# Optimization experiments

Hardware: AMD Instinct MI355X
Metric: run time of the kernel (lower is better)

The kernel has to match this reference:

```python
import jax, jax.numpy as jnp
import numpy as np

B, S, D, H = 2, 2048, 1024, 16
DH = D // H


def setup_inputs() -> dict:
    key = jax.random.key(0)
    ks = jax.random.split(key, 12)
    sc = 1.0 / np.sqrt(D)
    return {
        "query": jax.random.normal(ks[0], (B, S, D), jnp.float32),
        "key": jax.random.normal(ks[1], (B, S, D), jnp.float32),
        "value": jax.random.normal(ks[2], (B, S, D), jnp.float32),
        "key_mask": jax.random.randint(ks[3], (B, S), 0, 2, jnp.int32),
        "Wq": jax.random.normal(ks[4], (D, D), jnp.float32) * sc,
        "bq": jnp.zeros((D,), jnp.float32),
        "Wk": jax.random.normal(ks[5], (D, D), jnp.float32) * sc,
        "bk": jnp.zeros((D,), jnp.float32),
        "Wv": jax.random.normal(ks[6], (D, D), jnp.float32) * sc,
        "bv": jnp.zeros((D,), jnp.float32),
        "Wo": jax.random.normal(ks[7], (D, D), jnp.float32) * sc,
        "bo": jnp.zeros((D,), jnp.float32),
    }


def _shape(x):
    # (B, L, D) -> (B, H, L, DH)
    return x.reshape(B, -1, H, DH).transpose(0, 2, 1, 3)


def reference(query, key, value, key_mask, Wq, bq, Wk, bk, Wv, bv, Wo, bo):
    # linear projections (torch Linear: x @ W.T + b)
    q = _shape(query @ Wq.T + bq)  # (B,H,S,DH)
    k = _shape(key @ Wk.T + bk)
    v = _shape(value @ Wv.T + bv)

    q = q / jnp.sqrt(jnp.asarray(DH, q.dtype))
    scores = jnp.einsum("bhqd,bhkd->bhqk", q, k)  # (B,H,S,S)

    pad = (key_mask == 0)[:, None, None, :]  # (B,1,1,K)
    scores = jnp.where(pad, jnp.asarray(-1e18, scores.dtype), scores)
    attn = jax.nn.softmax(scores, axis=-1)
    attn = jnp.where(pad, jnp.asarray(0.0, attn.dtype), attn)
    # dropout p=0.0 (eval) -> identity

    ctx = jnp.einsum("bhqk,bhkd->bhqd", attn, v)
    ctx = ctx.transpose(0, 2, 1, 3).reshape(B, -1, D)  # unshape
    output = ctx @ Wo.T + bo
    return (output, attn)
```

## Files before the change

kernel.cpp:

```cpp
#include <hip/hip_runtime.h>

#define B_  2
#define S_  2048
#define D_  1024
#define H_  16
#define DH_ 64

typedef _Float16 f16;
typedef f16   f16x2 __attribute__((ext_vector_type(2)));
typedef f16   f16x4 __attribute__((ext_vector_type(4)));
typedef f16   f16x8 __attribute__((ext_vector_type(8)));
typedef float f32x4 __attribute__((ext_vector_type(4)));
typedef float f32x16 __attribute__((ext_vector_type(16)));

static __device__ __forceinline__ f16x8 ldsm8(const f16* p) {
    return *reinterpret_cast<const f16x8*>(p);
}

static __device__ __forceinline__ int swz(int row, int byteInRow) {
    return row * 128 + (byteInRow ^ ((row & 7) << 4));
}

static __device__ __forceinline__ void gll16(const void* g, void* l) {
    __builtin_amdgcn_global_load_lds(
        (const __attribute__((address_space(1))) void*)g,
        (__attribute__((address_space(3))) void*)l, 16, 0, 0);
}

static __device__ __forceinline__ unsigned pk16(float a, float b) {
    return __builtin_bit_cast(unsigned, __builtin_amdgcn_cvt_pkrtz(a, b));
}

__global__ __launch_bounds__(256)
void qkv_gemm(const float* __restrict__ Aq, const float* __restrict__ Ak,
              const float* __restrict__ Av,
              const float* __restrict__ Wq, const float* __restrict__ Wk,
              const float* __restrict__ Wv,
              const float* __restrict__ bq, const float* __restrict__ bk,
              const float* __restrict__ bv,
              f16* __restrict__ qo, f16* __restrict__ ko, f16* __restrict__ vo,
              float qscale)
{
    constexpr int K = 1024, N = 1024;
    __shared__ __align__(16) f16 As[128][40];
    __shared__ __align__(16) f16 Bs[128][40];
    const int z = blockIdx.z;
    const float* A    = z == 0 ? Aq : z == 1 ? Ak : Av;
    const float* W    = z == 0 ? Wq : z == 1 ? Wk : Wv;
    const float* bias = z == 0 ? bq : z == 1 ? bk : bv;
    const float scale = z == 0 ? qscale : 1.0f;

    const int t  = threadIdx.x;
    const int bm = blockIdx.y * 128;
    const int bn = blockIdx.x * 128;
    const int w  = t >> 6, l = t & 63;
    const int wr = w >> 1, wc = w & 1;
    const int lr = l & 15, lg = l >> 4;

    f32x4 acc[4][4];
    #pragma unroll
    for (int m = 0; m < 4; ++m)
        #pragma unroll
        for (int n = 0; n < 4; ++n)
            acc[m][n] = (f32x4){0.f, 0.f, 0.f, 0.f};

    for (int kt = 0; kt < K / 32; ++kt) {
        #pragma unroll
        for (int i = 0; i < 4; ++i) {
            int idx = t + i * 256;
            int row = idx >> 3, g = idx & 7;
            float4 v = *reinterpret_cast<const float4*>(A + (size_t)(bm + row) * K + kt * 32 + g * 4);
            alignas(8) f16 hh[4] = {(f16)v.x, (f16)v.y, (f16)v.z, (f16)v.w};
            *reinterpret_cast<uint2*>(&As[row][g * 4]) = *reinterpret_cast<uint2*>(hh);
        }
        #pragma unroll
        for (int i = 0; i < 4; ++i) {
            int idx = t + i * 256;
            int row = idx >> 3, g = idx & 7;
            float4 v = *reinterpret_cast<const float4*>(W + (size_t)(bn + row) * K + kt * 32 + g * 4);
            alignas(8) f16 hh[4] = {(f16)v.x, (f16)v.y, (f16)v.z, (f16)v.w};
            *reinterpret_cast<uint2*>(&Bs[row][g * 4]) = *reinterpret_cast<uint2*>(hh);
        }
        __syncthreads();

        f16x8 af[4], bfv[4];
        #pragma unroll
        for (int m = 0; m < 4; ++m) af[m]  = ldsm8(&As[wr * 64 + m * 16 + lr][lg * 8]);
        #pragma unroll
        for (int n = 0; n < 4; ++n) bfv[n] = ldsm8(&Bs[wc * 64 + n * 16 + lr][lg * 8]);
        #pragma unroll
        for (int m = 0; m < 4; ++m)
            #pragma unroll
            for (int n = 0; n < 4; ++n)
                acc[m][n] = __builtin_amdgcn_mfma_f32_16x16x32_f16(af[m], bfv[n], acc[m][n], 0, 0, 0);
        __syncthreads();
    }

    #pragma unroll
    for (int m = 0; m < 4; ++m) {
        #pragma unroll
        for (int n = 0; n < 4; ++n) {
            int col = bn + wc * 64 + n * 16 + lr;
            float bb = bias[col];
            if (z == 2) {
                int row0 = bm + wr * 64 + m * 16 + lg * 4;
                int b = row0 >> 11, s = row0 & 2047;
                int hh_ = col >> 6, d = col & 63;
                alignas(8) f16 hv[4];
                #pragma unroll
                for (int j = 0; j < 4; ++j)
                    hv[j] = (f16)(acc[m][n][j] + bb);
                *reinterpret_cast<uint2*>(vo +
                    (((size_t)(b * 16 + hh_) * 64 + d) * 2048 + s)) =
                    *reinterpret_cast<uint2*>(hv);
            } else {
                f16* Cp = z == 0 ? qo : ko;
                #pragma unroll
                for (int j = 0; j < 4; ++j) {
                    int row = bm + wr * 64 + m * 16 + lg * 4 + j;
                    Cp[(size_t)row * N + col] = (f16)((acc[m][n][j] + bb) * scale);
                }
            }
        }
    }
}

__global__ __launch_bounds__(256)
void gemm_out(const f16* __restrict__ A, const float* __restrict__ W,
              const float* __restrict__ bias, float* __restrict__ Cp)
{
    constexpr int K = 1024, N = 1024;
    __shared__ __align__(16) f16 As[128][40];
    __shared__ __align__(16) f16 Bs[128][40];
    const int t  = threadIdx.x;
    const int bm = blockIdx.y * 128;
    const int bn = blockIdx.x * 128;
    const int w  = t >> 6, l = t & 63;
    const int wr = w >> 1, wc = w & 1;
    const int lr = l & 15, lg = l >> 4;

    f32x4 acc[4][4];
    #pragma unroll
    for (int m = 0; m < 4; ++m)
        #pragma unroll
        for (int n = 0; n < 4; ++n)
            acc[m][n] = (f32x4){0.f, 0.f, 0.f, 0.f};

    for (int kt = 0; kt < K / 32; ++kt) {
        #pragma unroll
        for (int i = 0; i < 2; ++i) {
            int idx = t + i * 256;
            int row = idx >> 2, g = idx & 3;
            *reinterpret_cast<uint4*>(&As[row][g * 8]) =
                *reinterpret_cast<const uint4*>(A + (size_t)(bm + row) * K + kt * 32 + g * 8);
        }
        #pragma unroll
        for (int i = 0; i < 4; ++i) {
            int idx = t + i * 256;
            int row = idx >> 3, g = idx & 7;
            float4 v = *reinterpret_cast<const float4*>(W + (size_t)(bn + row) * K + kt * 32 + g * 4);
            alignas(8) f16 hh[4] = {(f16)v.x, (f16)v.y, (f16)v.z, (f16)v.w};
            *reinterpret_cast<uint2*>(&Bs[row][g * 4]) = *reinterpret_cast<uint2*>(hh);
        }
        __syncthreads();

        f16x8 af[4], bfv[4];
        #pragma unroll
        for (int m = 0; m < 4; ++m) af[m]  = ldsm8(&As[wr * 64 + m * 16 + lr][lg * 8]);
        #pragma unroll
        for (int n = 0; n < 4; ++n) bfv[n] = ldsm8(&Bs[wc * 64 + n * 16 + lr][lg * 8]);
        #pragma unroll
        for (int m = 0; m < 4; ++m)
            #pragma unroll
            for (int n = 0; n < 4; ++n)
                acc[m][n] = __builtin_amdgcn_mfma_f32_16x16x32_f16(af[m], bfv[n], acc[m][n], 0, 0, 0);
        __syncthreads();
    }

    #pragma unroll
    for (int m = 0; m < 4; ++m) {
        #pragma unroll
        for (int n = 0; n < 4; ++n) {
            int col = bn + wc * 64 + n * 16 + lr;
            float bb = bias[col];
            #pragma unroll
            for (int j = 0; j < 4; ++j) {
                int row = bm + wr * 64 + m * 16 + lg * 4 + j;
                Cp[(size_t)row * N + col] = acc[m][n][j] + bb;
            }
        }
    }
}

__global__ __launch_bounds__(256, 3)
void attn_fused(const f16* __restrict__ qh, const f16* __restrict__ khp,
                const f16* __restrict__ vtg, const int* __restrict__ kmask,
                float* __restrict__ attn_out, f16* __restrict__ ch)
{
    __shared__ __align__(16) f16 ksd[2][64 * 64];
    __shared__ __align__(16) f16 vsd[2][64 * 64];
    __shared__ __align__(16) f16 ps[128][76];
    __shared__ float linv_s[128];
    __shared__ unsigned mbits[64];

    const int t  = threadIdx.x;
    const int w  = t >> 6, l = t & 63, lo = l & 31, hi = l >> 5;
    const bool H1 = (hi == 1);

    const int bid  = blockIdx.x;
    const int xcd  = bid & 7;
    const int slot = bid >> 3;
    const int bh   = (xcd << 2) | (slot >> 4);
    const int qt   = slot & 15;
    const int b    = bh >> 4;
    const int h    = bh & 15;
    const int q0   = qt * 128;
    const int row  = q0 + w * 32 + lo;
    const int lrow = w * 32 + lo;

    f16x8 qf[4];
    {
        const f16* qb = qh + (size_t)(b * S_ + row) * D_ + h * DH_ + hi * 8;
        #pragma unroll
        for (int c = 0; c < 4; ++c) qf[c] = *reinterpret_cast<const f16x8*>(qb + c * 16);
    }

    #pragma unroll
    for (int r = 0; r < 8; ++r) {
        int ktm = w * 8 + r;
        int mkv = kmask[b * S_ + ktm * 64 + l];
        unsigned long long bl = __ballot(mkv != 0);
        if (l == 0) {
            mbits[ktm * 2]     = (unsigned)bl;
            mbits[ktm * 2 + 1] = (unsigned)(bl >> 32);
        }
    }
    asm volatile("s_waitcnt vmcnt(0)" ::: "memory");

    const int r8 = l >> 3, l8 = l & 7;
    const int xorc8 = (l8 ^ r8) * 8;
    const f16* kgb = khp + (size_t)b * S_ * D_ + h * DH_;
    const f16* vgb = vtg + (size_t)(bh * 64) * S_;

    auto stageK128 = [&](int slot2, int jt) {
        char* tb = slot2 ? (char*)&vsd[0][0] : (char*)&ksd[0][0];
        #pragma unroll
        for (int i = 0; i < 4; ++i) {
            int rr = w * 32 + i * 8 + r8;
            gll16(kgb + (size_t)(jt * 128 + rr) * D_ + xorc8,
                  tb + w * 4096 + i * 1024);
        }
    };
    auto stageK = [&](int buf, int kt) {
        #pragma unroll
        for (int i = 0; i < 2; ++i) {
            int rr = i * 32 + w * 8 + r8;
            gll16(kgb + (size_t)(kt * 64 + rr) * D_ + xorc8,
                  (char*)ksd + buf * 8192 + i * 4096 + w * 1024);
        }
    };
    auto stageV = [&](int buf, int kt) {
        #pragma unroll
        for (int i = 0; i < 2; ++i) {
            int rr = i * 32 + w * 8 + r8;
            gll16(vgb + (size_t)rr * S_ + kt * 64 + xorc8,
                  (char*)vsd + buf * 8192 + i * 4096 + w * 1024);
        }
    };

    stageK128(0, 0);
    asm volatile("s_waitcnt vmcnt(0) lgkmcnt(0)" ::: "memory");
    __builtin_amdgcn_s_barrier();

    float ls0 = 0.f, ls1 = 0.f;
    for (int jt = 0; jt < 16; ++jt) {
        if (jt + 1 < 16) stageK128((jt + 1) & 1, jt + 1);
        const char* tb = (jt & 1) ? (const char*)&vsd[0][0] : (const char*)&ksd[0][0];

        #pragma unroll
        for (int h4 = 0; h4 < 4; ++h4) {
            f32x16 s;
            #pragma unroll
            for (int i = 0; i < 16; ++i) s[i] = 0.f;
            #pragma unroll
            for (int c = 0; c < 4; ++c) {
                f16x8 kf = *reinterpret_cast<const f16x8*>(
                    tb + swz(h4 * 32 + lo, c * 32 + hi * 16));
                s = __builtin_amdgcn_mfma_f32_32x32x16_f16(kf, qf[c], s, 0, 0, 0);
            }
            const unsigned m = mbits[jt * 4 + h4] >> (hi * 4);
            #pragma unroll
            for (int q4 = 0; q4 < 4; ++q4)
                #pragma unroll
                for (int j = 0; j < 4; ++j) {
                    float e = __builtin_amdgcn_exp2f(s[q4 * 4 + j]);
                    float z = ((m >> (q4 * 8 + j)) & 1) ? e : 0.0f;
                    if (q4 & 1) ls1 += z; else ls0 += z;
                }
        }
        asm volatile("s_waitcnt vmcnt(0)" ::: "memory");
        __builtin_amdgcn_s_barrier();
    }

    float ls = ls0 + ls1;
    ls += __shfl_xor(ls, 32, 64);
    const float invl = 1.0f / ls;
    if (hi == 0) linv_s[lrow] = invl;

    stageK(0, 0); stageV(0, 0);
    asm volatile("s_waitcnt vmcnt(0) lgkmcnt(0)" ::: "memory");
    __builtin_amdgcn_s_barrier();

    f32x16 oc0, oc1;
    #pragma unroll
    for (int i = 0; i < 16; ++i) { oc0[i] = 0.f; oc1[i] = 0.f; }

    const int rseg  = t & 15;
    const int rrow0 = t >> 4;
    float* abase = attn_out + ((size_t)bh * S_ + q0) * S_;

    for (int kt = 0; kt < 32; ++kt) {
        if (kt + 1 < 32) {
            stageK((kt + 1) & 1, kt + 1);
            stageV((kt + 1) & 1, kt + 1);
        }
        const int cur = kt & 1;

        #pragma unroll
        for (int h2 = 0; h2 < 2; ++h2) {
            f32x16 s;
            #pragma unroll
            for (int i = 0; i < 16; ++i) s[i] = 0.f;
            #pragma unroll
            for (int c = 0; c < 4; ++c) {
                f16x8 kf = *reinterpret_cast<const f16x8*>(
                    (const char*)ksd + cur * 8192 + swz(lo + h2 * 32, c * 32 + hi * 16));
                s = __builtin_amdgcn_mfma_f32_32x32x16_f16(kf, qf[c], s, 0, 0, 0);
            }

            const unsigned m = mbits[kt * 2 + h2] >> (hi * 4);
            float p[16];
            #pragma unroll
            for (int q4 = 0; q4 < 4; ++q4)
                #pragma unroll
                for (int j = 0; j < 4; ++j) {
                    float e = __builtin_amdgcn_exp2f(s[q4 * 4 + j]);
                    p[q4 * 4 + j] = ((m >> (q4 * 8 + j)) & 1) ? e : 0.0f;
                }

            unsigned wa4[4], wb4[4];
            #pragma unroll
            for (int q4 = 0; q4 < 4; ++q4) {
                wa4[q4] = pk16(p[q4 * 4 + 0], p[q4 * 4 + 1]);
                wb4[q4] = pk16(p[q4 * 4 + 2], p[q4 * 4 + 3]);
                uint2 ww = {wa4[q4], wb4[q4]};
                *reinterpret_cast<uint2*>(&ps[lrow][h2 * 32 + q4 * 8 + hi * 4]) = ww;
            }

            #pragma unroll
            for (int cc = 0; cc < 2; ++cc) {
                const int c2 = h2 * 2 + cc, base = cc * 2;
                unsigned a0 = wa4[base], a1 = wa4[base + 1];
                unsigned b0 = wb4[base], b1 = wb4[base + 1];
                unsigned sa = H1 ? a0 : a1;
                unsigned sb = H1 ? b0 : b1;
                unsigned ra = (unsigned)__shfl_xor((int)sa, 32, 64);
                unsigned rb = (unsigned)__shfl_xor((int)sb, 32, 64);
                unsigned oa = H1 ? a1 : a0;
                unsigned ob = H1 ? b1 : b0;
                uint4 bw = H1 ? (uint4){ra, rb, oa, ob} : (uint4){oa, ob, ra, rb};
                f16x8 pf = __builtin_bit_cast(f16x8, bw);

                f16x8 va0 = *reinterpret_cast<const f16x8*>(
                    (const char*)vsd + cur * 8192 + swz(lo, c2 * 32 + hi * 16));
                f16x8 va1 = *reinterpret_cast<const f16x8*>(
                    (const char*)vsd + cur * 8192 + swz(lo + 32, c2 * 32 + hi * 16));
                oc0 = __builtin_amdgcn_mfma_f32_32x32x16_f16(va0, pf, oc0, 0, 0, 0);
                oc1 = __builtin_amdgcn_mfma_f32_32x32x16_f16(va1, pf, oc1, 0, 0, 0);
            }
        }

        asm volatile("s_waitcnt lgkmcnt(0)" ::: "memory");
        __builtin_amdgcn_s_barrier();

        #pragma unroll
        for (int ri = 0; ri < 8; ++ri) {
            int rr = ri * 16 + rrow0;
            f16x4 pv = *reinterpret_cast<const f16x4*>(&ps[rr][rseg * 4]);
            float li = linv_s[rr];
            f32x4 o = {(float)pv[0] * li, (float)pv[1] * li,
                       (float)pv[2] * li, (float)pv[3] * li};
            *reinterpret_cast<f32x4*>(abase + (size_t)rr * S_ + kt * 64 + rseg * 4) = o;
        }

        asm volatile("s_waitcnt vmcnt(8) lgkmcnt(0)" ::: "memory");
        __builtin_amdgcn_s_barrier();
    }

    f16* cb = ch + (size_t)(b * S_ + row) * D_ + h * DH_;
    #pragma unroll
    for (int q4 = 0; q4 < 4; ++q4) {
        int d0 = 8 * q4 + 4 * hi;
        f16x4 v0 = {(f16)(oc0[4 * q4 + 0] * invl), (f16)(oc0[4 * q4 + 1] * invl),
                    (f16)(oc0[4 * q4 + 2] * invl), (f16)(oc0[4 * q4 + 3] * invl)};
        *reinterpret_cast<f16x4*>(cb + d0) = v0;
        f16x4 v1 = {(f16)(oc1[4 * q4 + 0] * invl), (f16)(oc1[4 * q4 + 1] * invl),
                    (f16)(oc1[4 * q4 + 2] * invl), (f16)(oc1[4 * q4 + 3] * invl)};
        *reinterpret_cast<f16x4*>(cb + 32 + d0) = v1;
    }
}

extern "C" void kernel_launch(void* const* d_in, const int* in_sizes, int n_in,
                              void* d_out, int out_size, void* d_ws, size_t ws_size,
                              hipStream_t stream) {
    const float* query = (const float*)d_in[0];
    const float* key   = (const float*)d_in[1];
    const float* value = (const float*)d_in[2];
    const int*   kmask = (const int*)d_in[3];
    const float* Wq = (const float*)d_in[4];
    const float* bq = (const float*)d_in[5];
    const float* Wk = (const float*)d_in[6];
    const float* bk = (const float*)d_in[7];
    const float* Wv = (const float*)d_in[8];
    const float* bv = (const float*)d_in[9];
    const float* Wo = (const float*)d_in[10];
    const float* bo = (const float*)d_in[11];

    float* out  = (float*)d_out;
    float* attn = out + (size_t)B_ * S_ * D_;

    const size_t NE = (size_t)B_ * S_ * D_;
    f16* qhp = (f16*)d_ws;
    f16* khp = qhp + NE;
    f16* vtg = khp + NE;
    f16* chx = vtg + NE;

    const float qscale = 0.125f * 1.44269504088896340736f;

    qkv_gemm<<<dim3(8, 32, 3), 256, 0, stream>>>(query, key, value, Wq, Wk, Wv,
                                                 bq, bk, bv, qhp, khp, vtg, qscale);

    attn_fused<<<dim3(B_ * H_ * (S_ / 128)), 256, 0, stream>>>(qhp, khp, vtg, kmask,
                                                               attn, chx);

    gemm_out<<<dim3(8, 32), 256, 0, stream>>>(chx, Wo, bo, out);
}
```

Baseline: 296.1 us.

## Pre-convert weights to fp16 and use direct-to-LDS loads with K=64 tiles

Adds small kernels that convert the QKV and output-projection weights to fp16 in workspace buffers. The GEMMs then load weight tiles, and in gemm_out also activation tiles, with global_load_lds into swizzled LDS using a K step of 64, which halves the number of barriers and removes per-tile conversion. It also raises wave priority around the MFMA sections of the attention kernel. The cost is two extra launches, extra weight traffic, and reuse of the vtg and chx workspace buffers as scratch, which depends on the order of the kernels.

Result: no change. 298.3 us (+0.7%).

```diff
diff --git a/kernel.cpp b/kernel.cpp
--- a/kernel.cpp
+++ b/kernel.cpp
@@ -32,21 +32,43 @@
 }
 
 __global__ __launch_bounds__(256)
+void cvt_w3(const float* __restrict__ Wq, const float* __restrict__ Wk,
+            const float* __restrict__ Wv, f16* __restrict__ dst)
+{
+    size_t idx = ((size_t)blockIdx.x * 256 + threadIdx.x) * 8;
+    int z = (int)(idx >> 20);
+    size_t off = idx & 1048575;
+    const float* W = z == 0 ? Wq : z == 1 ? Wk : Wv;
+    float4 a = *reinterpret_cast<const float4*>(W + off);
+    float4 b = *reinterpret_cast<const float4*>(W + off + 4);
+    uint4 o = {pk16(a.x, a.y), pk16(a.z, a.w), pk16(b.x, b.y), pk16(b.z, b.w)};
+    *reinterpret_cast<uint4*>(dst + idx) = o;
+}
+
+__global__ __launch_bounds__(256)
+void cvt_w1(const float* __restrict__ Wo, f16* __restrict__ dst)
+{
+    size_t idx = ((size_t)blockIdx.x * 256 + threadIdx.x) * 8;
+    float4 a = *reinterpret_cast<const float4*>(Wo + idx);
+    float4 b = *reinterpret_cast<const float4*>(Wo + idx + 4);
+    uint4 o = {pk16(a.x, a.y), pk16(a.z, a.w), pk16(b.x, b.y), pk16(b.z, b.w)};
+    *reinterpret_cast<uint4*>(dst + idx) = o;
+}
+
+__global__ __launch_bounds__(256)
 void qkv_gemm(const float* __restrict__ Aq, const float* __restrict__ Ak,
-              const float* __restrict__ Av,
-              const float* __restrict__ Wq, const float* __restrict__ Wk,
-              const float* __restrict__ Wv,
+              const float* __restrict__ Av, const f16* __restrict__ W16,
               const float* __restrict__ bq, const float* __restrict__ bk,
               const float* __restrict__ bv,
               f16* __restrict__ qo, f16* __restrict__ ko, f16* __restrict__ vo,
               float qscale)
 {
     constexpr int K = 1024, N = 1024;
-    __shared__ __align__(16) f16 As[128][40];
-    __shared__ __align__(16) f16 Bs[128][40];
+    __shared__ __align__(16) f16 As[128][72];
+    __shared__ __align__(16) f16 Bs[128 * 64];
     const int z = blockIdx.z;
     const float* A    = z == 0 ? Aq : z == 1 ? Ak : Av;
-    const float* W    = z == 0 ? Wq : z == 1 ? Wk : Wv;
+    const f16*   W    = W16 + (size_t)z * 1024 * 1024;
     const float* bias = z == 0 ? bq : z == 1 ? bk : bv;
     const float scale = z == 0 ? qscale : 1.0f;
 
@@ -56,6 +78,8 @@
     const int w  = t >> 6, l = t & 63;
     const int wr = w >> 1, wc = w & 1;
     const int lr = l & 15, lg = l >> 4;
+    const int r8 = l >> 3, l8 = l & 7;
+    const int xorc8 = (l8 ^ r8) * 8;
 
     f32x4 acc[4][4];
     #pragma unroll
@@ -64,35 +88,40 @@
         for (int n = 0; n < 4; ++n)
             acc[m][n] = (f32x4){0.f, 0.f, 0.f, 0.f};
 
-    for (int kt = 0; kt < K / 32; ++kt) {
+    for (int km = 0; km < K / 64; ++km) {
         #pragma unroll
         for (int i = 0; i < 4; ++i) {
-            int idx = t + i * 256;
-            int row = idx >> 3, g = idx & 7;
-            float4 v = *reinterpret_cast<const float4*>(A + (size_t)(bm + row) * K + kt * 32 + g * 4);
-            alignas(8) f16 hh[4] = {(f16)v.x, (f16)v.y, (f16)v.z, (f16)v.w};
-            *reinterpret_cast<uint2*>(&As[row][g * 4]) = *reinterpret_cast<uint2*>(hh);
-        }
-        #pragma unroll
-        for (int i = 0; i < 4; ++i) {
-            int idx = t + i * 256;
-            int row = idx >> 3, g = idx & 7;
-            float4 v = *reinterpret_cast<const float4*>(W + (size_t)(bn + row) * K + kt * 32 + g * 4);
-            alignas(8) f16 hh[4] = {(f16)v.x, (f16)v.y, (f16)v.z, (f16)v.w};
-            *reinterpret_cast<uint2*>(&Bs[row][g * 4]) = *reinterpret_cast<uint2*>(hh);
-        }
-        __syncthreads();
-
-        f16x8 af[4], bfv[4];
-        #pragma unroll
-        for (int m = 0; m < 4; ++m) af[m]  = ldsm8(&As[wr * 64 + m * 16 + lr][lg * 8]);
-        #pragma unroll
-        for (int n = 0; n < 4; ++n) bfv[n] = ldsm8(&Bs[wc * 64 + n * 16 + lr][lg * 8]);
-        #pragma unroll
-        for (int m = 0; m < 4; ++m)
+            int rr = w * 32 + i * 8 + r8;
+            gll16(W + (size_t)(bn + rr) * K + km * 64 + xorc8,
+                  (char*)Bs + w * 4096 + i * 1024);
+        }
+        #pragma unroll
+        for (int i = 0; i < 8; ++i) {
+            int f = t + i * 256;
+            int row = f >> 4, c4 = (f & 15) * 4;
+            float4 v = *reinterpret_cast<const float4*>(A + (size_t)(bm + row) * K + km * 64 + c4);
+            uint2 hv = {pk16(v.x, v.y), pk16(v.z, v.w)};
+            *reinterpret_cast<uint2*>(&As[row][c4]) = hv;
+        }
+        asm volatile("s_waitcnt vmcnt(0) lgkmcnt(0)" ::: "memory");
+        __builtin_amdgcn_s_barrier();
+
+        #pragma unroll
+        for (int kk = 0; kk < 2; ++kk) {
+            f16x8 af[4], bfv[4];
+            #pragma unroll
+            for (int m = 0; m < 4; ++m)
+                af[m] = ldsm8(&As[wr * 64 + m * 16 + lr][kk * 32 + lg * 8]);
             #pragma unroll
             for (int n = 0; n < 4; ++n)
-                acc[m][n] = __builtin_amdgcn_mfma_f32_16x16x32_f16(af[m], bfv[n], acc[m][n], 0, 0, 0);
+                bfv[n] = *reinterpret_cast<const f16x8*>(
+                    (const char*)Bs + swz(wc * 64 + n * 16 + lr, kk * 64 + lg * 16));
+            #pragma unroll
+            for (int m = 0; m < 4; ++m)
+                #pragma unroll
+                for (int n = 0; n < 4; ++n)
+                    acc[m][n] = __builtin_amdgcn_mfma_f32_16x16x32_f16(af[m], bfv[n], acc[m][n], 0, 0, 0);
+        }
         __syncthreads();
     }
 
@@ -126,18 +155,20 @@
 }
 
 __global__ __launch_bounds__(256)
-void gemm_out(const f16* __restrict__ A, const float* __restrict__ W,
+void gemm_out(const f16* __restrict__ A, const f16* __restrict__ W16,
               const float* __restrict__ bias, float* __restrict__ Cp)
 {
     constexpr int K = 1024, N = 1024;
-    __shared__ __align__(16) f16 As[128][40];
-    __shared__ __align__(16) f16 Bs[128][40];
+    __shared__ __align__(16) f16 As[128 * 64];
+    __shared__ __align__(16) f16 Bs[128 * 64];
     const int t  = threadIdx.x;
     const int bm = blockIdx.y * 128;
     const int bn = blockIdx.x * 128;
     const int w  = t >> 6, l = t & 63;
     const int wr = w >> 1, wc = w & 1;
     const int lr = l & 15, lg = l >> 4;
+    const int r8 = l >> 3, l8 = l & 7;
+    const int xorc8 = (l8 ^ r8) * 8;
 
     f32x4 acc[4][4];
     #pragma unroll
@@ -146,34 +177,35 @@
         for (int n = 0; n < 4; ++n)
             acc[m][n] = (f32x4){0.f, 0.f, 0.f, 0.f};
 
-    for (int kt = 0; kt < K / 32; ++kt) {
-        #pragma unroll
-        for (int i = 0; i < 2; ++i) {
-            int idx = t + i * 256;
-            int row = idx >> 2, g = idx & 3;
-            *reinterpret_cast<uint4*>(&As[row][g * 8]) =
-                *reinterpret_cast<const uint4*>(A + (size_t)(bm + row) * K + kt * 32 + g * 8);
-        }
+    for (int km = 0; km < K / 64; ++km) {
         #pragma unroll
         for (int i = 0; i < 4; ++i) {
-            int idx = t + i * 256;
-            int row = idx >> 3, g = idx & 7;
-            float4 v = *reinterpret_cast<const float4*>(W + (size_t)(bn + row) * K + kt * 32 + g * 4);
-            alignas(8) f16 hh[4] = {(f16)v.x, (f16)v.y, (f16)v.z, (f16)v.w};
-            *reinterpret_cast<uint2*>(&Bs[row][g * 4]) = *reinterpret_cast<uint2*>(hh);
-        }
-        __syncthreads();
-
-        f16x8 af[4], bfv[4];
-        #pragma unroll
-        for (int m = 0; m < 4; ++m) af[m]  = ldsm8(&As[wr * 64 + m * 16 + lr][lg * 8]);
-        #pragma unroll
-        for (int n = 0; n < 4; ++n) bfv[n] = ldsm8(&Bs[wc * 64 + n * 16 + lr][lg * 8]);
-        #pragma unroll
-        for (int m = 0; m < 4; ++m)
+            int rr = w * 32 + i * 8 + r8;
+            gll16(A + (size_t)(bm + rr) * K + km * 64 + xorc8,
+                  (char*)As + w * 4096 + i * 1024);
+            gll16(W16 + (size_t)(bn + rr) * K + km * 64 + xorc8,
+                  (char*)Bs + w * 4096 + i * 1024);
+        }
+        asm volatile("s_waitcnt vmcnt(0)" ::: "memory");
+        __builtin_amdgcn_s_barrier();
+
+        #pragma unroll
+        for (int kk = 0; kk < 2; ++kk) {
+            f16x8 af[4], bfv[4];
+            #pragma unroll
+            for (int m = 0; m < 4; ++m)
+                af[m] = *reinterpret_cast<const f16x8*>(
+                    (const char*)As + swz(wr * 64 + m * 16 + lr, kk * 64 + lg * 16));
             #pragma unroll
             for (int n = 0; n < 4; ++n)
-                acc[m][n] = __builtin_amdgcn_mfma_f32_16x16x32_f16(af[m], bfv[n], acc[m][n], 0, 0, 0);
+                bfv[n] = *reinterpret_cast<const f16x8*>(
+                    (const char*)Bs + swz(wc * 64 + n * 16 + lr, kk * 64 + lg * 16));
+            #pragma unroll
+            for (int m = 0; m < 4; ++m)
+                #pragma unroll
+                for (int n = 0; n < 4; ++n)
+                    acc[m][n] = __builtin_amdgcn_mfma_f32_16x16x32_f16(af[m], bfv[n], acc[m][n], 0, 0, 0);
+        }
         __syncthreads();
     }
 
@@ -282,12 +314,14 @@
             f32x16 s;
             #pragma unroll
             for (int i = 0; i < 16; ++i) s[i] = 0.f;
+            __builtin_amdgcn_s_setprio(1);
             #pragma unroll
             for (int c = 0; c < 4; ++c) {
                 f16x8 kf = *reinterpret_cast<const f16x8*>(
                     tb + swz(h4 * 32 + lo, c * 32 + hi * 16));
                 s = __builtin_amdgcn_mfma_f32_32x32x16_f16(kf, qf[c], s, 0, 0, 0);
             }
+            __builtin_amdgcn_s_setprio(0);
             const unsigned m = mbits[jt * 4 + h4] >> (hi * 4);
             #pragma unroll
             for (int q4 = 0; q4 < 4; ++q4)
@@ -331,12 +365,14 @@
             f32x16 s;
             #pragma unroll
             for (int i = 0; i < 16; ++i) s[i] = 0.f;
+            __builtin_amdgcn_s_setprio(1);
             #pragma unroll
             for (int c = 0; c < 4; ++c) {
                 f16x8 kf = *reinterpret_cast<const f16x8*>(
                     (const char*)ksd + cur * 8192 + swz(lo + h2 * 32, c * 32 + hi * 16));
                 s = __builtin_amdgcn_mfma_f32_32x32x16_f16(kf, qf[c], s, 0, 0, 0);
             }
+            __builtin_amdgcn_s_setprio(0);
 
             const unsigned m = mbits[kt * 2 + h2] >> (hi * 4);
             float p[16];
@@ -375,8 +411,10 @@
                     (const char*)vsd + cur * 8192 + swz(lo, c2 * 32 + hi * 16));
                 f16x8 va1 = *reinterpret_cast<const f16x8*>(
                     (const char*)vsd + cur * 8192 + swz(lo + 32, c2 * 32 + hi * 16));
+                __builtin_amdgcn_s_setprio(1);
                 oc0 = __builtin_amdgcn_mfma_f32_32x32x16_f16(va0, pf, oc0, 0, 0, 0);
                 oc1 = __builtin_amdgcn_mfma_f32_32x32x16_f16(va1, pf, oc1, 0, 0, 0);
+                __builtin_amdgcn_s_setprio(0);
             }
         }
 
@@ -435,13 +473,20 @@
     f16* vtg = khp + NE;
     f16* chx = vtg + NE;
 
+    f16* Wqkv16 = chx;
+    f16* Wo16   = vtg;
+
     const float qscale = 0.125f * 1.44269504088896340736f;
 
-    qkv_gemm<<<dim3(8, 32, 3), 256, 0, stream>>>(query, key, value, Wq, Wk, Wv,
+    cvt_w3<<<dim3(1536), 256, 0, stream>>>(Wq, Wk, Wv, Wqkv16);
+
+    qkv_gemm<<<dim3(8, 32, 3), 256, 0, stream>>>(query, key, value, Wqkv16,
                                                  bq, bk, bv, qhp, khp, vtg, qscale);
 
     attn_fused<<<dim3(B_ * H_ * (S_ / 128)), 256, 0, stream>>>(qhp, khp, vtg, kmask,
                                                                attn, chx);
 
-    gemm_out<<<dim3(8, 32), 256, 0, stream>>>(chx, Wo, bo, out);
-}
+    cvt_w1<<<dim3(512), 256, 0, stream>>>(Wo, Wo16);
+
+    gemm_out<<<dim3(8, 32), 256, 0, stream>>>(chx, Wo16, bo, out);
+}
```
